# Optimization experiments

Measured on AMD Instinct MI355X. Metric: run time of the kernel, lower is better.

## Reference

```python
import jax, jax.numpy as jnp
import numpy as np

B, T, D = 2, 2048, 1024
H = 16
DK = D // H


def setup_inputs() -> dict:
    key = jax.random.key(0)
    ks = jax.random.split(key, 5)
    s = 1.0 / np.sqrt(D)
    return {
        "x": jax.random.normal(ks[0], (B, T, D), dtype=jnp.float32),
        "Wq": jax.random.normal(ks[1], (D, D), dtype=jnp.float32) * s,
        "bq": jnp.zeros((D,), dtype=jnp.float32),
        "Wk": jax.random.normal(ks[2], (D, D), dtype=jnp.float32) * s,
        "bk": jnp.zeros((D,), dtype=jnp.float32),
        "Wv": jax.random.normal(ks[3], (D, D), dtype=jnp.float32) * s,
        "bv": jnp.zeros((D,), dtype=jnp.float32),
        "Wo": jax.random.normal(ks[4], (D, D), dtype=jnp.float32) * s,
        "bo": jnp.zeros((D,), dtype=jnp.float32),
    }


def reference(x, Wq, bq, Wk, bk, Wv, bv, Wo, bo):
    # projections (torch Linear: x @ W.T + b; here W is stored as (in, out))
    Q = x @ Wq + bq  # (B,T,D)
    K = x @ Wk + bk
    V = x @ Wv + bv
    # split heads -> (B,H,T,dk)
    Q = Q.reshape(B, T, H, DK).transpose(0, 2, 1, 3)
    K = K.reshape(B, T, H, DK).transpose(0, 2, 1, 3)
    V = V.reshape(B, T, H, DK).transpose(0, 2, 1, 3)
    scale = 1.0 / jnp.sqrt(jnp.asarray(DK, dtype=x.dtype))
    scores = jnp.einsum("bhqd,bhkd->bhqk", Q, K) * scale  # (B,H,T,T)
    causal = jnp.tril(jnp.ones((T, T), dtype=bool))
    scores = jnp.where(causal, scores, -jnp.inf)
    weights = jax.nn.softmax(scores, axis=-1)
    # dropout is identity in eval mode
    context = jnp.einsum("bhqk,bhkd->bhqd", weights, V)
    context = context.transpose(0, 2, 1, 3).reshape(B, T, D)
    return context @ Wo + bo
```

## Files before the change

kernel.cpp:

```cpp
#include <hip/hip_runtime.h>
#include <hip/hip_bf16.h>

constexpr int Bc = 2;
constexpr int Tc = 2048;
constexpr int Mc = Bc * Tc;

typedef __attribute__((ext_vector_type(8))) __bf16 bf16x8;
typedef __attribute__((ext_vector_type(4))) __bf16 bf16x4;
typedef __attribute__((ext_vector_type(4))) float floatx4;

__device__ __forceinline__ void gl_lds16(const void* g, void* l) {
    __builtin_amdgcn_global_load_lds(
        (const __attribute__((address_space(1))) void*)g,
        (__attribute__((address_space(3))) void*)l, 16, 0, 0);
}

__global__ __launch_bounds__(256) void cvt_bf16(const float* __restrict__ in,
                                                __bf16* __restrict__ out, int n) {
    const int i = (blockIdx.x * 256 + threadIdx.x) * 4;
    if (i < n) {
        const float4 v = *(const float4*)(in + i);
        bf16x4 r;
        r[0] = (__bf16)v.x; r[1] = (__bf16)v.y;
        r[2] = (__bf16)v.z; r[3] = (__bf16)v.w;
        *(bf16x4*)(out + i) = r;
    }
}

__global__ __launch_bounds__(256) void wtrans_all(const float* __restrict__ Wq,
                                                  const float* __restrict__ Wk,
                                                  const float* __restrict__ Wv,
                                                  const float* __restrict__ Wo,
                                                  __bf16* __restrict__ Wqkv,
                                                  __bf16* __restrict__ Wot) {
    __shared__ float t[64][65];
    const int z = blockIdx.z;
    const float* W = (z == 0) ? Wq : (z == 1) ? Wk : (z == 2) ? Wv : Wo;
    __bf16* Wt = (z < 3) ? Wqkv + (size_t)z * 1024 * 1024 : Wot;
    const int k0 = blockIdx.y * 64, n0 = blockIdx.x * 64;
    const int c = threadIdx.x & 63, r0 = threadIdx.x >> 6;
#pragma unroll
    for (int i = 0; i < 16; ++i)
        t[r0 + i * 4][c] = W[(size_t)(k0 + r0 + i * 4) * 1024 + n0 + c];
    __syncthreads();
#pragma unroll
    for (int i = 0; i < 16; ++i) {
        const int r = r0 + i * 4;
        Wt[(size_t)(n0 + r) * 1024 + k0 + c] = (__bf16)t[c][r];
    }
}

template <int TN, bool BF16_OUT, bool FUSE_VT>
__global__ __launch_bounds__(256) void gemm_bt(const __bf16* __restrict__ A,
                                               const __bf16* __restrict__ Bt,
                                               const float* __restrict__ b0,
                                               const float* __restrict__ b1,
                                               const float* __restrict__ b2,
                                               void* __restrict__ Cv,
                                               __bf16* __restrict__ Vt,
                                               int K, int ldc) {
    constexpr int NI = TN / 32;
    __shared__ __bf16 As[128 * 32];
    __shared__ __bf16 Bs[TN * 32];
    const int tid = threadIdx.x, lane = tid & 63, wave = tid >> 6;
    const int wm = wave & 1, wn = wave >> 1;
    const int bm = blockIdx.y * 128, bn = blockIdx.x * TN;
    const __bf16* Ab = A + (size_t)bm * K;
    const __bf16* Bb = Bt + (size_t)bn * K;
    const int quad = lane >> 4, tm = lane & 15;

    floatx4 acc[4][NI] = {};

    for (int k0 = 0; k0 < K; k0 += 32) {
#pragma unroll
        for (int i = 0; i < 2; ++i) {
            const int s = i * 256 + tid;
            gl_lds16(Ab + (size_t)(s >> 2) * K + k0 + (s & 3) * 8, As + s * 8);
        }
        if (TN == 128) {
#pragma unroll
            for (int i = 0; i < 2; ++i) {
                const int s = i * 256 + tid;
                gl_lds16(Bb + (size_t)(s >> 2) * K + k0 + (s & 3) * 8, Bs + s * 8);
            }
        } else {
            const int s = tid;
            gl_lds16(Bb + (size_t)(s >> 2) * K + k0 + (s & 3) * 8, Bs + s * 8);
        }
        __syncthreads();
        bf16x8 af[4], bfv[NI];
#pragma unroll
        for (int mi = 0; mi < 4; ++mi)
            af[mi] = *(const bf16x8*)(As + (wm * 64 + mi * 16 + tm) * 32 + quad * 8);
#pragma unroll
        for (int ni = 0; ni < NI; ++ni)
            bfv[ni] = *(const bf16x8*)(Bs + (wn * (TN / 2) + ni * 16 + tm) * 32 + quad * 8);
#pragma unroll
        for (int mi = 0; mi < 4; ++mi)
#pragma unroll
            for (int ni = 0; ni < NI; ++ni)
                acc[mi][ni] = __builtin_amdgcn_mfma_f32_16x16x32_bf16(
                    af[mi], bfv[ni], acc[mi][ni], 0, 0, 0);
        __syncthreads();
    }

#pragma unroll
    for (int ni = 0; ni < NI; ++ni) {
        const int gc = bn + wn * (TN / 2) + ni * 16 + tm;
        const float bias = (gc < 1024) ? b0[gc]
                         : (gc < 2048) ? b1[gc - 1024]
                                       : b2[gc - 2048];
#pragma unroll
        for (int mi = 0; mi < 4; ++mi) {
            const int gr0 = bm + wm * 64 + mi * 16 + quad * 4;
            if (FUSE_VT && gc >= 2048) {
                bf16x4 pv;
#pragma unroll
                for (int r = 0; r < 4; ++r) pv[r] = (__bf16)(acc[mi][ni][r] + bias);
                const int bb = gr0 >> 11, tloc = gr0 & 2047;
                const int hh = (gc - 2048) >> 6, dd = gc & 63;
                *(bf16x4*)(Vt + ((size_t)(bb * 16 + hh) * 64 + dd) * 2048 + tloc) = pv;
            } else if (BF16_OUT) {
#pragma unroll
                for (int r = 0; r < 4; ++r)
                    ((__bf16*)Cv)[(size_t)(gr0 + r) * ldc + gc] =
                        (__bf16)(acc[mi][ni][r] + bias);
            } else {
#pragma unroll
                for (int r = 0; r < 4; ++r)
                    ((float*)Cv)[(size_t)(gr0 + r) * ldc + gc] =
                        acc[mi][ni][r] + bias;
            }
        }
    }
}

__global__ __launch_bounds__(256) void attn_mfma(const __bf16* __restrict__ QK,
                                                 const __bf16* __restrict__ Vt,
                                                 __bf16* __restrict__ ctx) {
    constexpr float Cf = 0.18033688011112042f;
    constexpr float NEG = -1e30f;

    __shared__ __bf16 Ks[2][64 * 64];
    __shared__ __bf16 Vts[2][64 * 64];

    const int tid = threadIdx.x, lane = tid & 63, w = tid >> 6;
    const int c = lane & 15, quad = lane >> 4;
    const int bh = blockIdx.y, b = bh >> 4, h = bh & 15;
    const int ta = blockIdx.x, tb = 31 - ta;
    const int tg[2] = {tb, ta};
    const int nk = tb + 1;

    const __bf16* Qb = QK + (size_t)(b * Tc) * 2048 + h * 64;
    const __bf16* Kb = Qb + 1024;
    const __bf16* Vtb = Vt + (size_t)bh * 64 * 2048;

    bf16x8 qf0[2], qf1[2];
#pragma unroll
    for (int g = 0; g < 2; ++g) {
        const __bf16* qr = Qb + (size_t)(tg[g] * 64 + w * 16 + c) * 2048;
        qf0[g] = *(const bf16x8*)(qr + quad * 8);
        qf1[g] = *(const bf16x8*)(qr + 32 + quad * 8);
    }

    float m[2] = {NEG, NEG}, l[2] = {0.f, 0.f};
    floatx4 oa[2][4] = {};

#pragma unroll
    for (int i = 0; i < 2; ++i) {
        const int s = i * 256 + tid;
        const int row = s >> 3;
        const int lc = (s & 7) ^ (row & 7);
        gl_lds16(Kb + (size_t)row * 2048 + lc * 8, &Ks[0][s * 8]);
        gl_lds16(Vtb + (size_t)row * 2048 + lc * 8, &Vts[0][s * 8]);
    }
    __syncthreads();

    for (int kt = 0; kt < nk; ++kt) {
        const int buf = kt & 1;
        if (kt + 1 < nk) {
            const int k0n = (kt + 1) * 64;
#pragma unroll
            for (int i = 0; i < 2; ++i) {
                const int s = i * 256 + tid;
                const int row = s >> 3;
                const int lc = (s & 7) ^ (row & 7);
                gl_lds16(Kb + (size_t)(k0n + row) * 2048 + lc * 8, &Ks[buf ^ 1][s * 8]);
                gl_lds16(Vtb + (size_t)row * 2048 + k0n + lc * 8, &Vts[buf ^ 1][s * 8]);
            }
        }
        const __bf16* ks = Ks[buf];
        const __bf16* vs = Vts[buf];
        const bool actA = (kt <= ta);

        float sv[2][4][4];
#pragma unroll
        for (int ni = 0; ni < 4; ++ni) {
            const int krow = ni * 16 + c;
            const int sw = krow & 7;
            const bf16x8 kb0 = *(const bf16x8*)(ks + krow * 64 + (quad ^ sw) * 8);
            const bf16x8 kb1 = *(const bf16x8*)(ks + krow * 64 + ((4 + quad) ^ sw) * 8);
            {
                floatx4 a = {};
                a = __builtin_amdgcn_mfma_f32_16x16x32_bf16(kb0, qf0[0], a, 0, 0, 0);
                a = __builtin_amdgcn_mfma_f32_16x16x32_bf16(kb1, qf1[0], a, 0, 0, 0);
#pragma unroll
                for (int r = 0; r < 4; ++r) sv[0][ni][r] = a[r];
            }
            if (actA) {
                floatx4 a = {};
                a = __builtin_amdgcn_mfma_f32_16x16x32_bf16(kb0, qf0[1], a, 0, 0, 0);
                a = __builtin_amdgcn_mfma_f32_16x16x32_bf16(kb1, qf1[1], a, 0, 0, 0);
#pragma unroll
                for (int r = 0; r < 4; ++r) sv[1][ni][r] = a[r];
            }
        }

        bf16x8 pb[2][2];
        float alpha[2];
#pragma unroll
        for (int g = 0; g < 2; ++g) {
            if (g == 1 && !actA) continue;
            if (kt == tg[g]) {
#pragma unroll
                for (int ni = 0; ni < 4; ++ni)
#pragma unroll
                    for (int r = 0; r < 4; ++r)
                        if (ni * 16 + quad * 4 + r > w * 16 + c) sv[g][ni][r] = NEG;
            }
            float rm = sv[g][0][0];
#pragma unroll
            for (int ni = 0; ni < 4; ++ni)
#pragma unroll
                for (int r = 0; r < 4; ++r) rm = fmaxf(rm, sv[g][ni][r]);
            rm = fmaxf(rm, __shfl_xor(rm, 16));
            rm = fmaxf(rm, __shfl_xor(rm, 32));
            const float nm = fmaxf(m[g], rm);
            alpha[g] = __builtin_exp2f((m[g] - nm) * Cf);
            const float nmc = -nm * Cf;
            float sum = 0.f;
#pragma unroll
            for (int ni = 0; ni < 4; ++ni)
#pragma unroll
                for (int r = 0; r < 4; ++r) {
                    const float p = __builtin_exp2f(fmaf(sv[g][ni][r], Cf, nmc));
                    sv[g][ni][r] = p;
                    sum += p;
                }
            sum += __shfl_xor(sum, 16);
            sum += __shfl_xor(sum, 32);
            m[g] = nm;
            l[g] = l[g] * alpha[g] + sum;
#pragma unroll
            for (int pr = 0; pr < 2; ++pr)
#pragma unroll
                for (int j = 0; j < 4; ++j) {
                    pb[g][pr][j] = (__bf16)sv[g][pr * 2][j];
                    pb[g][pr][4 + j] = (__bf16)sv[g][pr * 2 + 1][j];
                }
#pragma unroll
            for (int di = 0; di < 4; ++di)
#pragma unroll
                for (int r = 0; r < 4; ++r) oa[g][di][r] *= alpha[g];
        }

#pragma unroll
        for (int di = 0; di < 4; ++di) {
            const int vrow = di * 16 + c;
            const int sw2 = vrow & 7;
#pragma unroll
            for (int pr = 0; pr < 2; ++pr) {
                const int lc0 = (2 * (pr * 2) + (quad >> 1)) ^ sw2;
                const int lc1 = (2 * (pr * 2 + 1) + (quad >> 1)) ^ sw2;
                const bf16x4 va =
                    *(const bf16x4*)(vs + vrow * 64 + lc0 * 8 + (quad & 1) * 4);
                const bf16x4 vb =
                    *(const bf16x4*)(vs + vrow * 64 + lc1 * 8 + (quad & 1) * 4);
                bf16x8 vf;
#pragma unroll
                for (int j = 0; j < 4; ++j) { vf[j] = va[j]; vf[4 + j] = vb[j]; }
                oa[0][di] = __builtin_amdgcn_mfma_f32_16x16x32_bf16(
                    vf, pb[0][pr], oa[0][di], 0, 0, 0);
                if (actA)
                    oa[1][di] = __builtin_amdgcn_mfma_f32_16x16x32_bf16(
                        vf, pb[1][pr], oa[1][di], 0, 0, 0);
            }
        }
        __syncthreads();
    }

#pragma unroll
    for (int g = 0; g < 2; ++g) {
        const float inv = 1.f / l[g];
        __bf16* cp = ctx + (size_t)(b * Tc + tg[g] * 64 + w * 16 + c) * 1024 +
                     h * 64 + quad * 4;
#pragma unroll
        for (int di = 0; di < 4; ++di) {
            bf16x4 rv;
#pragma unroll
            for (int r = 0; r < 4; ++r) rv[r] = (__bf16)(oa[g][di][r] * inv);
            *(bf16x4*)(cp + di * 16) = rv;
        }
    }
}

extern "C" void kernel_launch(void* const* d_in, const int* in_sizes, int n_in,
                              void* d_out, int out_size, void* d_ws, size_t ws_size,
                              hipStream_t stream) {
    const float* x  = (const float*)d_in[0];
    const float* Wq = (const float*)d_in[1];
    const float* bq = (const float*)d_in[2];
    const float* Wk = (const float*)d_in[3];
    const float* bk = (const float*)d_in[4];
    const float* Wv = (const float*)d_in[5];
    const float* bv = (const float*)d_in[6];
    const float* Wo = (const float*)d_in[7];
    const float* bo = (const float*)d_in[8];

    __bf16* xb   = (__bf16*)d_ws;
    __bf16* Wqkv = xb + (size_t)Mc * 1024;
    __bf16* Wot  = Wqkv + (size_t)3072 * 1024;
    __bf16* QKb  = Wot + (size_t)1024 * 1024;
    __bf16* Vtw  = QKb + (size_t)Mc * 2048;
    __bf16* ctxb = Vtw + (size_t)32 * 64 * 2048;

    cvt_bf16<<<4096, 256, 0, stream>>>(x, xb, Mc * 1024);
    wtrans_all<<<dim3(16, 16, 4), 256, 0, stream>>>(Wq, Wk, Wv, Wo, Wqkv, Wot);

    gemm_bt<128, true, true><<<dim3(24, 32), 256, 0, stream>>>(
        xb, Wqkv, bq, bk, bv, QKb, Vtw, 1024, 2048);

    attn_mfma<<<dim3(16, 32), 256, 0, stream>>>(QKb, Vtw, ctxb);

    gemm_bt<64, false, false><<<dim3(16, 32), 256, 0, stream>>>(
        ctxb, Wot, bo, bo, bo, d_out, nullptr, 1024, 1024);
}
```

Before: 209.6 us.

## Split paired-tile attention into one query tile per block; merge prep kernels

The attention kernel no longer pairs query tiles ta and 31-ta in one block. It launches 32x32 blocks, each handling one query tile chosen by a rotated index, and precomputes the LDS offsets and global pointers for the K/V loads. The x conversion and the weight transposes are merged into one prep launch to save a kernel launch. This doubles the block count and simplifies the inner loop, but loses the load balance from pairing and the reuse of K/V tiles across two query tiles, so K/V traffic grows.

```diff
diff --git a/kernel.cpp b/kernel.cpp
--- a/kernel.cpp
+++ b/kernel.cpp
@@ -15,30 +15,35 @@
         (__attribute__((address_space(3))) void*)l, 16, 0, 0);
 }
 
-__global__ __launch_bounds__(256) void cvt_bf16(const float* __restrict__ in,
-                                                __bf16* __restrict__ out, int n) {
-    const int i = (blockIdx.x * 256 + threadIdx.x) * 4;
-    if (i < n) {
-        const float4 v = *(const float4*)(in + i);
-        bf16x4 r;
-        r[0] = (__bf16)v.x; r[1] = (__bf16)v.y;
-        r[2] = (__bf16)v.z; r[3] = (__bf16)v.w;
-        *(bf16x4*)(out + i) = r;
-    }
-}
-
-__global__ __launch_bounds__(256) void wtrans_all(const float* __restrict__ Wq,
-                                                  const float* __restrict__ Wk,
-                                                  const float* __restrict__ Wv,
-                                                  const float* __restrict__ Wo,
-                                                  __bf16* __restrict__ Wqkv,
-                                                  __bf16* __restrict__ Wot) {
+__global__ __launch_bounds__(256) void prep_all(const float* __restrict__ x,
+                                                const float* __restrict__ Wq,
+                                                const float* __restrict__ Wk,
+                                                const float* __restrict__ Wv,
+                                                const float* __restrict__ Wo,
+                                                __bf16* __restrict__ xb,
+                                                __bf16* __restrict__ Wqkv,
+                                                __bf16* __restrict__ Wot) {
+    const int z = blockIdx.z;
+    const int tid = threadIdx.x;
+    if (z >= 4) {
+        const int lb = blockIdx.y * 16 + blockIdx.x;
+        const size_t base = ((size_t)(z - 4) * 256 + lb) * 4096;
+#pragma unroll
+        for (int it = 0; it < 4; ++it) {
+            const size_t i = base + (size_t)(it * 256 + tid) * 4;
+            const float4 v = *(const float4*)(x + i);
+            bf16x4 r;
+            r[0] = (__bf16)v.x; r[1] = (__bf16)v.y;
+            r[2] = (__bf16)v.z; r[3] = (__bf16)v.w;
+            *(bf16x4*)(xb + i) = r;
+        }
+        return;
+    }
     __shared__ float t[64][65];
-    const int z = blockIdx.z;
     const float* W = (z == 0) ? Wq : (z == 1) ? Wk : (z == 2) ? Wv : Wo;
     __bf16* Wt = (z < 3) ? Wqkv + (size_t)z * 1024 * 1024 : Wot;
     const int k0 = blockIdx.y * 64, n0 = blockIdx.x * 64;
-    const int c = threadIdx.x & 63, r0 = threadIdx.x >> 6;
+    const int c = tid & 63, r0 = tid >> 6;
 #pragma unroll
     for (int i = 0; i < 16; ++i)
         t[r0 + i * 4][c] = W[(size_t)(k0 + r0 + i * 4) * 1024 + n0 + c];
@@ -147,160 +152,154 @@
     const int tid = threadIdx.x, lane = tid & 63, w = tid >> 6;
     const int c = lane & 15, quad = lane >> 4;
     const int bh = blockIdx.y, b = bh >> 4, h = bh & 15;
-    const int ta = blockIdx.x, tb = 31 - ta;
-    const int tg[2] = {tb, ta};
-    const int nk = tb + 1;
+    const int qt = ((int)blockIdx.x + (int)blockIdx.y) & 31;
+    const int nk = qt + 1;
 
     const __bf16* Qb = QK + (size_t)(b * Tc) * 2048 + h * 64;
     const __bf16* Kb = Qb + 1024;
     const __bf16* Vtb = Vt + (size_t)bh * 64 * 2048;
 
-    bf16x8 qf0[2], qf1[2];
-#pragma unroll
-    for (int g = 0; g < 2; ++g) {
-        const __bf16* qr = Qb + (size_t)(tg[g] * 64 + w * 16 + c) * 2048;
-        qf0[g] = *(const bf16x8*)(qr + quad * 8);
-        qf1[g] = *(const bf16x8*)(qr + 32 + quad * 8);
-    }
-
-    float m[2] = {NEG, NEG}, l[2] = {0.f, 0.f};
-    floatx4 oa[2][4] = {};
-
-#pragma unroll
-    for (int i = 0; i < 2; ++i) {
-        const int s = i * 256 + tid;
-        const int row = s >> 3;
-        const int lc = (s & 7) ^ (row & 7);
-        gl_lds16(Kb + (size_t)row * 2048 + lc * 8, &Ks[0][s * 8]);
-        gl_lds16(Vtb + (size_t)row * 2048 + lc * 8, &Vts[0][s * 8]);
-    }
+    const __bf16* qr = Qb + (size_t)(qt * 64 + w * 16 + c) * 2048;
+    const bf16x8 qf0 = *(const bf16x8*)(qr + quad * 8);
+    const bf16x8 qf1 = *(const bf16x8*)(qr + 32 + quad * 8);
+
+    float m = NEG, l = 0.f;
+    floatx4 oa[4] = {};
+
+    const int sw = c & 7;
+    int koff0[4], koff1[4];
+#pragma unroll
+    for (int ni = 0; ni < 4; ++ni) {
+        const int krow = ni * 16 + c;
+        koff0[ni] = krow * 64 + (quad ^ sw) * 8;
+        koff1[ni] = krow * 64 + ((4 + quad) ^ sw) * 8;
+    }
+    int voff0[4][2], voff1[4][2];
+#pragma unroll
+    for (int di = 0; di < 4; ++di) {
+        const int vrow = di * 16 + c;
+#pragma unroll
+        for (int pr = 0; pr < 2; ++pr) {
+            const int lc0 = (4 * pr + (quad >> 1)) ^ sw;
+            const int lc1 = (4 * pr + 2 + (quad >> 1)) ^ sw;
+            voff0[di][pr] = vrow * 64 + lc0 * 8 + (quad & 1) * 4;
+            voff1[di][pr] = vrow * 64 + lc1 * 8 + (quad & 1) * 4;
+        }
+    }
+
+    const int srow = tid >> 3;
+    const int slc = (tid & 7) ^ (srow & 7);
+    const __bf16* kg0 = Kb + (size_t)srow * 2048 + slc * 8;
+    const __bf16* kg1 = kg0 + (size_t)32 * 2048;
+    const __bf16* vg0 = Vtb + (size_t)srow * 2048 + slc * 8;
+    const __bf16* vg1 = vg0 + (size_t)32 * 2048;
+    __bf16* kd0 = &Ks[0][tid * 8];
+    __bf16* vd0 = &Vts[0][tid * 8];
+
+    gl_lds16(kg0, kd0);
+    gl_lds16(kg1, kd0 + 256 * 8);
+    gl_lds16(vg0, vd0);
+    gl_lds16(vg1, vd0 + 256 * 8);
+    kg0 += 64 * 2048; kg1 += 64 * 2048;
+    vg0 += 64; vg1 += 64;
     __syncthreads();
 
     for (int kt = 0; kt < nk; ++kt) {
         const int buf = kt & 1;
         if (kt + 1 < nk) {
-            const int k0n = (kt + 1) * 64;
-#pragma unroll
-            for (int i = 0; i < 2; ++i) {
-                const int s = i * 256 + tid;
-                const int row = s >> 3;
-                const int lc = (s & 7) ^ (row & 7);
-                gl_lds16(Kb + (size_t)(k0n + row) * 2048 + lc * 8, &Ks[buf ^ 1][s * 8]);
-                gl_lds16(Vtb + (size_t)row * 2048 + k0n + lc * 8, &Vts[buf ^ 1][s * 8]);
-            }
+            __bf16* kd = &Ks[buf ^ 1][tid * 8];
+            __bf16* vd = &Vts[buf ^ 1][tid * 8];
+            gl_lds16(kg0, kd);
+            gl_lds16(kg1, kd + 256 * 8);
+            gl_lds16(vg0, vd);
+            gl_lds16(vg1, vd + 256 * 8);
+            kg0 += 64 * 2048; kg1 += 64 * 2048;
+            vg0 += 64; vg1 += 64;
         }
         const __bf16* ks = Ks[buf];
         const __bf16* vs = Vts[buf];
-        const bool actA = (kt <= ta);
-
-        float sv[2][4][4];
+
+        float sv[4][4];
 #pragma unroll
         for (int ni = 0; ni < 4; ++ni) {
-            const int krow = ni * 16 + c;
-            const int sw = krow & 7;
-            const bf16x8 kb0 = *(const bf16x8*)(ks + krow * 64 + (quad ^ sw) * 8);
-            const bf16x8 kb1 = *(const bf16x8*)(ks + krow * 64 + ((4 + quad) ^ sw) * 8);
-            {
-                floatx4 a = {};
-                a = __builtin_amdgcn_mfma_f32_16x16x32_bf16(kb0, qf0[0], a, 0, 0, 0);
-                a = __builtin_amdgcn_mfma_f32_16x16x32_bf16(kb1, qf1[0], a, 0, 0, 0);
-#pragma unroll
-                for (int r = 0; r < 4; ++r) sv[0][ni][r] = a[r];
-            }
-            if (actA) {
-                floatx4 a = {};
-                a = __builtin_amdgcn_mfma_f32_16x16x32_bf16(kb0, qf0[1], a, 0, 0, 0);
-                a = __builtin_amdgcn_mfma_f32_16x16x32_bf16(kb1, qf1[1], a, 0, 0, 0);
-#pragma unroll
-                for (int r = 0; r < 4; ++r) sv[1][ni][r] = a[r];
-            }
-        }
-
-        bf16x8 pb[2][2];
-        float alpha[2];
-#pragma unroll
-        for (int g = 0; g < 2; ++g) {
-            if (g == 1 && !actA) continue;
-            if (kt == tg[g]) {
-#pragma unroll
-                for (int ni = 0; ni < 4; ++ni)
-#pragma unroll
-                    for (int r = 0; r < 4; ++r)
-                        if (ni * 16 + quad * 4 + r > w * 16 + c) sv[g][ni][r] = NEG;
-            }
-            float rm = sv[g][0][0];
+            const bf16x8 kb0 = *(const bf16x8*)(ks + koff0[ni]);
+            const bf16x8 kb1 = *(const bf16x8*)(ks + koff1[ni]);
+            floatx4 a = {};
+            a = __builtin_amdgcn_mfma_f32_16x16x32_bf16(kb0, qf0, a, 0, 0, 0);
+            a = __builtin_amdgcn_mfma_f32_16x16x32_bf16(kb1, qf1, a, 0, 0, 0);
+#pragma unroll
+            for (int r = 0; r < 4; ++r) sv[ni][r] = a[r];
+        }
+
+        if (kt == qt) {
 #pragma unroll
             for (int ni = 0; ni < 4; ++ni)
 #pragma unroll
-                for (int r = 0; r < 4; ++r) rm = fmaxf(rm, sv[g][ni][r]);
-            rm = fmaxf(rm, __shfl_xor(rm, 16));
-            rm = fmaxf(rm, __shfl_xor(rm, 32));
-            const float nm = fmaxf(m[g], rm);
-            alpha[g] = __builtin_exp2f((m[g] - nm) * Cf);
-            const float nmc = -nm * Cf;
-            float sum = 0.f;
-#pragma unroll
-            for (int ni = 0; ni < 4; ++ni)
-#pragma unroll
-                for (int r = 0; r < 4; ++r) {
-                    const float p = __builtin_exp2f(fmaf(sv[g][ni][r], Cf, nmc));
-                    sv[g][ni][r] = p;
-                    sum += p;
-                }
-            sum += __shfl_xor(sum, 16);
-            sum += __shfl_xor(sum, 32);
-            m[g] = nm;
-            l[g] = l[g] * alpha[g] + sum;
-#pragma unroll
-            for (int pr = 0; pr < 2; ++pr)
-#pragma unroll
-                for (int j = 0; j < 4; ++j) {
-                    pb[g][pr][j] = (__bf16)sv[g][pr * 2][j];
-                    pb[g][pr][4 + j] = (__bf16)sv[g][pr * 2 + 1][j];
-                }
-#pragma unroll
-            for (int di = 0; di < 4; ++di)
-#pragma unroll
-                for (int r = 0; r < 4; ++r) oa[g][di][r] *= alpha[g];
-        }
-
+                for (int r = 0; r < 4; ++r)
+                    if (ni * 16 + quad * 4 + r > w * 16 + c) sv[ni][r] = NEG;
+        }
+        float rm = sv[0][0];
+#pragma unroll
+        for (int ni = 0; ni < 4; ++ni)
+#pragma unroll
+            for (int r = 0; r < 4; ++r) rm = fmaxf(rm, sv[ni][r]);
+        rm = fmaxf(rm, __shfl_xor(rm, 16));
+        rm = fmaxf(rm, __shfl_xor(rm, 32));
+        const float nm = fmaxf(m, rm);
+        const float alpha = __builtin_exp2f((m - nm) * Cf);
+        const float nmc = -nm * Cf;
+        float sum = 0.f;
+#pragma unroll
+        for (int ni = 0; ni < 4; ++ni)
+#pragma unroll
+            for (int r = 0; r < 4; ++r) {
+                const float p = __builtin_exp2f(fmaf(sv[ni][r], Cf, nmc));
+                sv[ni][r] = p;
+                sum += p;
+            }
+        sum += __shfl_xor(sum, 16);
+        sum += __shfl_xor(sum, 32);
+        m = nm;
+        l = l * alpha + sum;
+
+        bf16x8 pb[2];
+#pragma unroll
+        for (int pr = 0; pr < 2; ++pr)
+#pragma unroll
+            for (int j = 0; j < 4; ++j) {
+                pb[pr][j] = (__bf16)sv[pr * 2][j];
+                pb[pr][4 + j] = (__bf16)sv[pr * 2 + 1][j];
+            }
+
+#pragma unroll
+        for (int di = 0; di < 4; ++di)
+#pragma unroll
+            for (int r = 0; r < 4; ++r) oa[di][r] *= alpha;
 #pragma unroll
         for (int di = 0; di < 4; ++di) {
-            const int vrow = di * 16 + c;
-            const int sw2 = vrow & 7;
 #pragma unroll
             for (int pr = 0; pr < 2; ++pr) {
-                const int lc0 = (2 * (pr * 2) + (quad >> 1)) ^ sw2;
-                const int lc1 = (2 * (pr * 2 + 1) + (quad >> 1)) ^ sw2;
-                const bf16x4 va =
-                    *(const bf16x4*)(vs + vrow * 64 + lc0 * 8 + (quad & 1) * 4);
-                const bf16x4 vb =
-                    *(const bf16x4*)(vs + vrow * 64 + lc1 * 8 + (quad & 1) * 4);
+                const bf16x4 va = *(const bf16x4*)(vs + voff0[di][pr]);
+                const bf16x4 vb = *(const bf16x4*)(vs + voff1[di][pr]);
                 bf16x8 vf;
 #pragma unroll
                 for (int j = 0; j < 4; ++j) { vf[j] = va[j]; vf[4 + j] = vb[j]; }
-                oa[0][di] = __builtin_amdgcn_mfma_f32_16x16x32_bf16(
-                    vf, pb[0][pr], oa[0][di], 0, 0, 0);
-                if (actA)
-                    oa[1][di] = __builtin_amdgcn_mfma_f32_16x16x32_bf16(
-                        vf, pb[1][pr], oa[1][di], 0, 0, 0);
+                oa[di] = __builtin_amdgcn_mfma_f32_16x16x32_bf16(
+                    vf, pb[pr], oa[di], 0, 0, 0);
             }
         }
         __syncthreads();
     }
 
-#pragma unroll
-    for (int g = 0; g < 2; ++g) {
-        const float inv = 1.f / l[g];
-        __bf16* cp = ctx + (size_t)(b * Tc + tg[g] * 64 + w * 16 + c) * 1024 +
-                     h * 64 + quad * 4;
-#pragma unroll
-        for (int di = 0; di < 4; ++di) {
-            bf16x4 rv;
-#pragma unroll
-            for (int r = 0; r < 4; ++r) rv[r] = (__bf16)(oa[g][di][r] * inv);
-            *(bf16x4*)(cp + di * 16) = rv;
-        }
+    const float inv = 1.f / l;
+    __bf16* cp = ctx + (size_t)(b * Tc + qt * 64 + w * 16 + c) * 1024 +
+                 h * 64 + quad * 4;
+#pragma unroll
+    for (int di = 0; di < 4; ++di) {
+        bf16x4 rv;
+#pragma unroll
+        for (int r = 0; r < 4; ++r) rv[r] = (__bf16)(oa[di][r] * inv);
+        *(bf16x4*)(cp + di * 16) = rv;
     }
 }
 
@@ -324,13 +323,13 @@
     __bf16* Vtw  = QKb + (size_t)Mc * 2048;
     __bf16* ctxb = Vtw + (size_t)32 * 64 * 2048;
 
-    cvt_bf16<<<4096, 256, 0, stream>>>(x, xb, Mc * 1024);
-    wtrans_all<<<dim3(16, 16, 4), 256, 0, stream>>>(Wq, Wk, Wv, Wo, Wqkv, Wot);
+    prep_all<<<dim3(16, 16, 8), 256, 0, stream>>>(x, Wq, Wk, Wv, Wo,
+                                                  xb, Wqkv, Wot);
 
     gemm_bt<128, true, true><<<dim3(24, 32), 256, 0, stream>>>(
         xb, Wqkv, bq, bk, bv, QKb, Vtw, 1024, 2048);
 
-    attn_mfma<<<dim3(16, 32), 256, 0, stream>>>(QKb, Vtw, ctxb);
+    attn_mfma<<<dim3(32, 32), 256, 0, stream>>>(QKb, Vtw, ctxb);
 
     gemm_bt<64, false, false><<<dim3(16, 32), 256, 0, stream>>>(
         ctxb, Wot, bo, bo, bo, d_out, nullptr, 1024, 1024);
```

Result: no change. 211.2 us (+0.8%).

## Split attention KV range across two blocks and merge with combine kernel

Applied to the files above, without the earlier changes.

Each causal-paired attention block now handles only every other KV tile (even or odd), which doubles the grid from 512 to 1024 blocks. Each block writes unnormalized partial outputs plus row max and sum, and a new combine kernel merges the two halves with log-sum-exp weighting. The input cast and the weight transpose are also fused into one prep launch, and the LDS swizzle offsets are hoisted out of the loop. This raises occupancy and parallelism on a 256-CU device, at the cost of an extra launch, partial-output traffic, and bf16 rounding of the unnormalized partials.

```diff
diff --git a/kernel.cpp b/kernel.cpp
--- a/kernel.cpp
+++ b/kernel.cpp
@@ -15,30 +15,35 @@
         (__attribute__((address_space(3))) void*)l, 16, 0, 0);
 }
 
-__global__ __launch_bounds__(256) void cvt_bf16(const float* __restrict__ in,
-                                                __bf16* __restrict__ out, int n) {
-    const int i = (blockIdx.x * 256 + threadIdx.x) * 4;
-    if (i < n) {
-        const float4 v = *(const float4*)(in + i);
-        bf16x4 r;
-        r[0] = (__bf16)v.x; r[1] = (__bf16)v.y;
-        r[2] = (__bf16)v.z; r[3] = (__bf16)v.w;
-        *(bf16x4*)(out + i) = r;
-    }
-}
-
-__global__ __launch_bounds__(256) void wtrans_all(const float* __restrict__ Wq,
-                                                  const float* __restrict__ Wk,
-                                                  const float* __restrict__ Wv,
-                                                  const float* __restrict__ Wo,
-                                                  __bf16* __restrict__ Wqkv,
-                                                  __bf16* __restrict__ Wot) {
+__global__ __launch_bounds__(256) void prep_all(const float* __restrict__ x,
+                                                const float* __restrict__ Wq,
+                                                const float* __restrict__ Wk,
+                                                const float* __restrict__ Wv,
+                                                const float* __restrict__ Wo,
+                                                __bf16* __restrict__ xb,
+                                                __bf16* __restrict__ Wqkv,
+                                                __bf16* __restrict__ Wot) {
+    const int z = blockIdx.z;
+    const int tid = threadIdx.x;
+    if (z >= 4) {
+        const int lb = blockIdx.y * 16 + blockIdx.x;
+        const size_t base = ((size_t)(z - 4) * 256 + lb) * 4096;
+#pragma unroll
+        for (int it = 0; it < 4; ++it) {
+            const size_t i = base + (size_t)(it * 256 + tid) * 4;
+            const float4 v = *(const float4*)(x + i);
+            bf16x4 r;
+            r[0] = (__bf16)v.x; r[1] = (__bf16)v.y;
+            r[2] = (__bf16)v.z; r[3] = (__bf16)v.w;
+            *(bf16x4*)(xb + i) = r;
+        }
+        return;
+    }
     __shared__ float t[64][65];
-    const int z = blockIdx.z;
     const float* W = (z == 0) ? Wq : (z == 1) ? Wk : (z == 2) ? Wv : Wo;
     __bf16* Wt = (z < 3) ? Wqkv + (size_t)z * 1024 * 1024 : Wot;
     const int k0 = blockIdx.y * 64, n0 = blockIdx.x * 64;
-    const int c = threadIdx.x & 63, r0 = threadIdx.x >> 6;
+    const int c = tid & 63, r0 = tid >> 6;
 #pragma unroll
     for (int i = 0; i < 16; ++i)
         t[r0 + i * 4][c] = W[(size_t)(k0 + r0 + i * 4) * 1024 + n0 + c];
@@ -135,9 +140,10 @@
     }
 }
 
-__global__ __launch_bounds__(256) void attn_mfma(const __bf16* __restrict__ QK,
+__global__ __launch_bounds__(256) void attn_part(const __bf16* __restrict__ QK,
                                                  const __bf16* __restrict__ Vt,
-                                                 __bf16* __restrict__ ctx) {
+                                                 __bf16* __restrict__ Opart,
+                                                 float* __restrict__ Lm) {
     constexpr float Cf = 0.18033688011112042f;
     constexpr float NEG = -1e30f;
 
@@ -147,9 +153,9 @@
     const int tid = threadIdx.x, lane = tid & 63, w = tid >> 6;
     const int c = lane & 15, quad = lane >> 4;
     const int bh = blockIdx.y, b = bh >> 4, h = bh & 15;
-    const int ta = blockIdx.x, tb = 31 - ta;
+    const int p = (int)blockIdx.x >> 1, half = (int)blockIdx.x & 1;
+    const int ta = p, tb = 31 - p;
     const int tg[2] = {tb, ta};
-    const int nk = tb + 1;
 
     const __bf16* Qb = QK + (size_t)(b * Tc) * 2048 + h * 64;
     const __bf16* Kb = Qb + 1024;
@@ -166,28 +172,53 @@
     float m[2] = {NEG, NEG}, l[2] = {0.f, 0.f};
     floatx4 oa[2][4] = {};
 
-#pragma unroll
-    for (int i = 0; i < 2; ++i) {
-        const int s = i * 256 + tid;
-        const int row = s >> 3;
-        const int lc = (s & 7) ^ (row & 7);
-        gl_lds16(Kb + (size_t)row * 2048 + lc * 8, &Ks[0][s * 8]);
-        gl_lds16(Vtb + (size_t)row * 2048 + lc * 8, &Vts[0][s * 8]);
-    }
+    const int sw = c & 7;
+    int koff0[4], koff1[4];
+#pragma unroll
+    for (int ni = 0; ni < 4; ++ni) {
+        const int krow = ni * 16 + c;
+        koff0[ni] = krow * 64 + (quad ^ sw) * 8;
+        koff1[ni] = krow * 64 + ((4 + quad) ^ sw) * 8;
+    }
+    int voff0[4][2], voff1[4][2];
+#pragma unroll
+    for (int di = 0; di < 4; ++di) {
+        const int vrow = di * 16 + c;
+#pragma unroll
+        for (int pr = 0; pr < 2; ++pr) {
+            const int lc0 = (4 * pr + (quad >> 1)) ^ sw;
+            const int lc1 = (4 * pr + 2 + (quad >> 1)) ^ sw;
+            voff0[di][pr] = vrow * 64 + lc0 * 8 + (quad & 1) * 4;
+            voff1[di][pr] = vrow * 64 + lc1 * 8 + (quad & 1) * 4;
+        }
+    }
+
+    const int srow = tid >> 3;
+    const int slc = (tid & 7) ^ (srow & 7);
+    const __bf16* kg0 = Kb + (size_t)(half * 64 + srow) * 2048 + slc * 8;
+    const __bf16* kg1 = kg0 + (size_t)32 * 2048;
+    const __bf16* vg0 = Vtb + (size_t)srow * 2048 + half * 64 + slc * 8;
+    const __bf16* vg1 = vg0 + (size_t)32 * 2048;
+
+    gl_lds16(kg0, &Ks[0][tid * 8]);
+    gl_lds16(kg1, &Ks[0][tid * 8 + 2048]);
+    gl_lds16(vg0, &Vts[0][tid * 8]);
+    gl_lds16(vg1, &Vts[0][tid * 8 + 2048]);
+    kg0 += (size_t)128 * 2048; kg1 += (size_t)128 * 2048;
+    vg0 += 128; vg1 += 128;
     __syncthreads();
 
-    for (int kt = 0; kt < nk; ++kt) {
-        const int buf = kt & 1;
-        if (kt + 1 < nk) {
-            const int k0n = (kt + 1) * 64;
-#pragma unroll
-            for (int i = 0; i < 2; ++i) {
-                const int s = i * 256 + tid;
-                const int row = s >> 3;
-                const int lc = (s & 7) ^ (row & 7);
-                gl_lds16(Kb + (size_t)(k0n + row) * 2048 + lc * 8, &Ks[buf ^ 1][s * 8]);
-                gl_lds16(Vtb + (size_t)row * 2048 + k0n + lc * 8, &Vts[buf ^ 1][s * 8]);
-            }
+    int buf = 0;
+    for (int kt = half; kt <= tb; kt += 2) {
+        if (kt + 2 <= tb) {
+            __bf16* kd = &Ks[buf ^ 1][tid * 8];
+            __bf16* vd = &Vts[buf ^ 1][tid * 8];
+            gl_lds16(kg0, kd);
+            gl_lds16(kg1, kd + 2048);
+            gl_lds16(vg0, vd);
+            gl_lds16(vg1, vd + 2048);
+            kg0 += (size_t)128 * 2048; kg1 += (size_t)128 * 2048;
+            vg0 += 128; vg1 += 128;
         }
         const __bf16* ks = Ks[buf];
         const __bf16* vs = Vts[buf];
@@ -196,10 +227,8 @@
         float sv[2][4][4];
 #pragma unroll
         for (int ni = 0; ni < 4; ++ni) {
-            const int krow = ni * 16 + c;
-            const int sw = krow & 7;
-            const bf16x8 kb0 = *(const bf16x8*)(ks + krow * 64 + (quad ^ sw) * 8);
-            const bf16x8 kb1 = *(const bf16x8*)(ks + krow * 64 + ((4 + quad) ^ sw) * 8);
+            const bf16x8 kb0 = *(const bf16x8*)(ks + koff0[ni]);
+            const bf16x8 kb1 = *(const bf16x8*)(ks + koff1[ni]);
             {
                 floatx4 a = {};
                 a = __builtin_amdgcn_mfma_f32_16x16x32_bf16(kb0, qf0[0], a, 0, 0, 0);
@@ -243,9 +272,9 @@
             for (int ni = 0; ni < 4; ++ni)
 #pragma unroll
                 for (int r = 0; r < 4; ++r) {
-                    const float p = __builtin_exp2f(fmaf(sv[g][ni][r], Cf, nmc));
-                    sv[g][ni][r] = p;
-                    sum += p;
+                    const float pp = __builtin_exp2f(fmaf(sv[g][ni][r], Cf, nmc));
+                    sv[g][ni][r] = pp;
+                    sum += pp;
                 }
             sum += __shfl_xor(sum, 16);
             sum += __shfl_xor(sum, 32);
@@ -266,16 +295,10 @@
 
 #pragma unroll
         for (int di = 0; di < 4; ++di) {
-            const int vrow = di * 16 + c;
-            const int sw2 = vrow & 7;
 #pragma unroll
             for (int pr = 0; pr < 2; ++pr) {
-                const int lc0 = (2 * (pr * 2) + (quad >> 1)) ^ sw2;
-                const int lc1 = (2 * (pr * 2 + 1) + (quad >> 1)) ^ sw2;
-                const bf16x4 va =
-                    *(const bf16x4*)(vs + vrow * 64 + lc0 * 8 + (quad & 1) * 4);
-                const bf16x4 vb =
-                    *(const bf16x4*)(vs + vrow * 64 + lc1 * 8 + (quad & 1) * 4);
+                const bf16x4 va = *(const bf16x4*)(vs + voff0[di][pr]);
+                const bf16x4 vb = *(const bf16x4*)(vs + voff1[di][pr]);
                 bf16x8 vf;
 #pragma unroll
                 for (int j = 0; j < 4; ++j) { vf[j] = va[j]; vf[4 + j] = vb[j]; }
@@ -287,20 +310,59 @@
             }
         }
         __syncthreads();
+        buf ^= 1;
     }
 
 #pragma unroll
     for (int g = 0; g < 2; ++g) {
-        const float inv = 1.f / l[g];
-        __bf16* cp = ctx + (size_t)(b * Tc + tg[g] * 64 + w * 16 + c) * 1024 +
-                     h * 64 + quad * 4;
+        const size_t pbase = ((size_t)(bh * 32 + tg[g]) * 2 + half);
+        if (quad == 0) {
+            float* lm = Lm + pbase * 128 + w * 16 + c;
+            lm[0] = m[g];
+            lm[64] = l[g];
+        }
+        __bf16* Op = Opart + pbase * 4096 + (size_t)(w * 16 + c) * 64;
 #pragma unroll
         for (int di = 0; di < 4; ++di) {
             bf16x4 rv;
 #pragma unroll
-            for (int r = 0; r < 4; ++r) rv[r] = (__bf16)(oa[g][di][r] * inv);
-            *(bf16x4*)(cp + di * 16) = rv;
-        }
+            for (int r = 0; r < 4; ++r) rv[r] = (__bf16)(oa[g][di][r]);
+            *(bf16x4*)(Op + di * 16 + quad * 4) = rv;
+        }
+    }
+}
+
+__global__ __launch_bounds__(256) void attn_combine(const __bf16* __restrict__ Opart,
+                                                    const float* __restrict__ Lm,
+                                                    __bf16* __restrict__ ctx) {
+    constexpr float Cf = 0.18033688011112042f;
+    const int tid = threadIdx.x;
+    const int qt = blockIdx.x, bh = blockIdx.y;
+    const int b = bh >> 4, h = bh & 15;
+    const int q = tid >> 2, ds = (tid & 3) * 16;
+    const size_t pb0 = (size_t)(bh * 32 + qt) * 2;
+    const size_t pb1 = pb0 + 1;
+
+    const float m0 = Lm[pb0 * 128 + q], l0 = Lm[pb0 * 128 + 64 + q];
+    const float m1 = Lm[pb1 * 128 + q], l1 = Lm[pb1 * 128 + 64 + q];
+    const float M = fmaxf(m0, m1);
+    const float w0 = __builtin_exp2f((m0 - M) * Cf);
+    const float w1 = __builtin_exp2f((m1 - M) * Cf);
+    const float inv = 1.f / (w0 * l0 + w1 * l1);
+    const float s0 = w0 * inv, s1 = w1 * inv;
+
+    const __bf16* O0 = Opart + pb0 * 4096 + (size_t)q * 64 + ds;
+    const __bf16* O1 = Opart + pb1 * 4096 + (size_t)q * 64 + ds;
+    __bf16* cp = ctx + (size_t)(b * Tc + qt * 64 + q) * 1024 + h * 64 + ds;
+#pragma unroll
+    for (int u = 0; u < 2; ++u) {
+        const bf16x8 a = *(const bf16x8*)(O0 + u * 8);
+        const bf16x8 bb = *(const bf16x8*)(O1 + u * 8);
+        bf16x8 o;
+#pragma unroll
+        for (int j = 0; j < 8; ++j)
+            o[j] = (__bf16)(s0 * (float)a[j] + s1 * (float)bb[j]);
+        *(bf16x8*)(cp + u * 8) = o;
     }
 }
 
@@ -317,20 +379,23 @@
     const float* Wo = (const float*)d_in[7];
     const float* bo = (const float*)d_in[8];
 
-    __bf16* xb   = (__bf16*)d_ws;
-    __bf16* Wqkv = xb + (size_t)Mc * 1024;
-    __bf16* Wot  = Wqkv + (size_t)3072 * 1024;
-    __bf16* QKb  = Wot + (size_t)1024 * 1024;
-    __bf16* Vtw  = QKb + (size_t)Mc * 2048;
-    __bf16* ctxb = Vtw + (size_t)32 * 64 * 2048;
-
-    cvt_bf16<<<4096, 256, 0, stream>>>(x, xb, Mc * 1024);
-    wtrans_all<<<dim3(16, 16, 4), 256, 0, stream>>>(Wq, Wk, Wv, Wo, Wqkv, Wot);
+    __bf16* xb    = (__bf16*)d_ws;
+    __bf16* Wqkv  = xb + (size_t)Mc * 1024;
+    __bf16* Wot   = Wqkv + (size_t)3072 * 1024;
+    __bf16* QKb   = Wot + (size_t)1024 * 1024;
+    __bf16* Vtw   = QKb + (size_t)Mc * 2048;
+    __bf16* ctxb  = Vtw + (size_t)32 * 64 * 2048;
+    __bf16* Opart = ctxb + (size_t)Mc * 1024;
+    float*  Lmbuf = (float*)(Opart + (size_t)32 * 32 * 2 * 4096);
+
+    prep_all<<<dim3(16, 16, 8), 256, 0, stream>>>(x, Wq, Wk, Wv, Wo,
+                                                  xb, Wqkv, Wot);
 
     gemm_bt<128, true, true><<<dim3(24, 32), 256, 0, stream>>>(
         xb, Wqkv, bq, bk, bv, QKb, Vtw, 1024, 2048);
 
-    attn_mfma<<<dim3(16, 32), 256, 0, stream>>>(QKb, Vtw, ctxb);
+    attn_part<<<dim3(32, 32), 256, 0, stream>>>(QKb, Vtw, Opart, Lmbuf);
+    attn_combine<<<dim3(32, 32), 256, 0, stream>>>(Opart, Lmbuf, ctxb);
 
     gemm_bt<64, false, false><<<dim3(16, 32), 256, 0, stream>>>(
         ctxb, Wot, bo, bo, bo, d_out, nullptr, 1024, 1024);
```

Result: slower. 222.7 us (+6.3%).
